# Kernel optimization log

Hardware: AMD Instinct MI355X
Metric: run time of the kernel (lower is better)

The kernel has to match this reference:

```python
import jax, jax.numpy as jnp
import numpy as np

N_NODES = 50000
N_EDGES = 400000
IN_F = 512
HID = 512      # 2 * out_features
OUT_F = 256
N_CELL = 1000
N_DIM = 128
N_SEL = 8192
N_C = 1024


def setup_inputs() -> dict:
    key = jax.random.key(0)
    ks = jax.random.split(key, 16)
    x = jax.random.normal(ks[0], (N_NODES, IN_F), dtype=jnp.float32)
    src = jax.random.randint(ks[1], (N_EDGES,), 0, N_NODES, dtype=jnp.int32)
    dst = jax.random.randint(ks[2], (N_EDGES,), 0, N_NODES, dtype=jnp.int32)
    x_indices = jax.random.randint(ks[3], (N_SEL,), 0, N_NODES, dtype=jnp.int32)
    c_indices = jax.random.randint(ks[4], (N_C,), 0, N_CELL, dtype=jnp.int32)
    s = lambda f: 1.0 / np.sqrt(f)
    W1 = jax.random.normal(ks[5], (IN_F, HID), dtype=jnp.float32) * s(IN_F)
    b1 = jnp.zeros((HID,), jnp.float32)
    W2 = jax.random.normal(ks[6], (HID, HID), dtype=jnp.float32) * s(HID)
    b2 = jnp.zeros((HID,), jnp.float32)
    W3 = jax.random.normal(ks[7], (HID, OUT_F), dtype=jnp.float32) * s(HID)
    b3 = jnp.zeros((OUT_F,), jnp.float32)
    Wp = jax.random.normal(ks[8], (OUT_F, N_DIM), dtype=jnp.float32) * s(OUT_F)
    bp = jnp.zeros((N_DIM,), jnp.float32)
    emb = jax.random.normal(ks[9], (N_CELL, N_DIM), dtype=jnp.float32)
    return {"x": x, "src": src, "dst": dst, "x_indices": x_indices,
            "c_indices": c_indices, "W1": W1, "b1": b1, "W2": W2, "b2": b2,
            "W3": W3, "b3": b3, "Wp": Wp, "bp": bp, "emb": emb}


def _degree_norms(src, dst, n):
    ones = jnp.ones(src.shape[0], jnp.float32)
    deg_out = jax.ops.segment_sum(ones, src, num_segments=n)
    deg_in = jax.ops.segment_sum(ones, dst, num_segments=n)
    ns = jnp.where(deg_out > 0, jax.lax.rsqrt(jnp.maximum(deg_out, 1.0)), 0.0)
    nd = jnp.where(deg_in > 0, jax.lax.rsqrt(jnp.maximum(deg_in, 1.0)), 0.0)
    return ns[:, None], nd[:, None]


def _gconv(h, src, dst, norm_src, norm_dst, W, b, n):
    # DGL GraphConv, norm='both': D_in^{-1/2} A D_out^{-1/2} H W + b
    msg = (h * norm_src)[src]                         # [E, F]
    agg = jax.ops.segment_sum(msg, dst, num_segments=n)
    return (agg * norm_dst) @ W + b


def reference(x, src, dst, x_indices, c_indices, W1, b1, W2, b2, W3, b3, Wp, bp, emb):
    n = x.shape[0]
    ns, nd = _degree_norms(src, dst, n)
    h = jax.nn.relu(_gconv(x, src, dst, ns, nd, W1, b1, n))
    h = jax.nn.relu(_gconv(h, src, dst, ns, nd, W2, b2, n))
    h = jax.nn.relu(_gconv(h, src, dst, ns, nd, W3, b3, n))
    enc = h[x_indices]                                # [N_SEL, OUT_F]
    proj = enc @ Wp + bp                              # Dropout in eval mode = identity
    e = emb[c_indices]                                # [N_C, N_DIM]
    return e @ proj.T                                 # [N_C, N_SEL]
```

## Files before the change

### kernel.cpp

```cpp
#include <hip/hip_runtime.h>

typedef unsigned int u32;
typedef unsigned short u16;

#define N_NODES 50000
#define N_EDGES 400000
#define IN_F 512
#define HID 512
#define OUT_F 256
#define N_CELL 1000
#define N_DIM 128
#define N_SEL 8192
#define N_C 1024
#define MPAD 50176

#define SCAN_B 256
#define SCAN_NB ((N_NODES + SCAN_B - 1) / SCAN_B)

typedef __bf16 bf16x8 __attribute__((ext_vector_type(8)));
typedef float f32x4 __attribute__((ext_vector_type(4)));

__device__ __forceinline__ u16 f2bf(float f) {
    u32 u = __builtin_bit_cast(u32, f);
    u32 r = (u + 0x7fffu + ((u >> 16) & 1u)) >> 16;
    return (u16)r;
}
__device__ __forceinline__ float bf2f(u32 bits16) {
    return __builtin_bit_cast(float, bits16 << 16);
}

__device__ __forceinline__ void async_copy16(const u16* g, u16* l) {
    __builtin_amdgcn_global_load_lds(
        (const __attribute__((address_space(1))) void*)g,
        (__attribute__((address_space(3))) void*)l, 16, 0, 0);
}


__global__ void degrees_kernel(const int* __restrict__ src, const int* __restrict__ dst,
                               int* __restrict__ degO, int* __restrict__ degI) {
    int e = blockIdx.x * 256 + threadIdx.x;
    if (e < N_EDGES) {
        atomicAdd(&degO[src[e]], 1);
        atomicAdd(&degI[dst[e]], 1);
    }
}

__global__ void scan_blocksum_kernel(const int* __restrict__ deg, int* __restrict__ bsum) {
    __shared__ int sh[SCAN_B];
    int i = blockIdx.x * SCAN_B + threadIdx.x;
    int v = (i < N_NODES) ? deg[i] : 0;
    sh[threadIdx.x] = v;
    __syncthreads();
    for (int off = SCAN_B / 2; off > 0; off >>= 1) {
        if (threadIdx.x < off) sh[threadIdx.x] += sh[threadIdx.x + off];
        __syncthreads();
    }
    if (threadIdx.x == 0) bsum[blockIdx.x] = sh[0];
}

__global__ void scan_bsum_kernel(const int* __restrict__ bsum, int* __restrict__ boff) {
    __shared__ int sh[SCAN_B];
    const int t = threadIdx.x;
    int v = (t < SCAN_NB) ? bsum[t] : 0;
    sh[t] = v;
    __syncthreads();
    for (int off = 1; off < SCAN_B; off <<= 1) {
        int u = (t >= off) ? sh[t - off] : 0;
        __syncthreads();
        sh[t] += u;
        __syncthreads();
    }
    if (t < SCAN_NB) boff[t] = sh[t] - v;
}

__global__ void scan_final_kernel(const int* __restrict__ deg, const int* __restrict__ boff,
                                  int* __restrict__ offs) {
    __shared__ int sh[SCAN_B];
    const int t = threadIdx.x;
    int i = blockIdx.x * SCAN_B + t;
    int v = (i < N_NODES) ? deg[i] : 0;
    sh[t] = v;
    __syncthreads();
    for (int off = 1; off < SCAN_B; off <<= 1) {
        int u = (t >= off) ? sh[t - off] : 0;
        __syncthreads();
        sh[t] += u;
        __syncthreads();
    }
    if (i < N_NODES) offs[i] = boff[blockIdx.x] + sh[t] - v;
    if (i == 0) offs[N_NODES] = N_EDGES;
}

__global__ void fill_csr_kernel(const int* __restrict__ src, const int* __restrict__ dst,
                                int* __restrict__ cursor, const int* __restrict__ offs,
                                int* __restrict__ csr) {
    int e = blockIdx.x * 256 + threadIdx.x;
    if (e < N_EDGES) {
        int d = dst[e];
        int slot = atomicAdd(&cursor[d], 1);
        csr[offs[d] + slot] = src[e];
    }
}

__global__ void norms_kernel(const int* __restrict__ degO, const int* __restrict__ degI,
                             float* __restrict__ ns, float* __restrict__ nd) {
    int i = blockIdx.x * 256 + threadIdx.x;
    if (i < N_NODES) {
        ns[i] = degO[i] > 0 ? rsqrtf((float)degO[i]) : 0.f;
        nd[i] = degI[i] > 0 ? rsqrtf((float)degI[i]) : 0.f;
    }
}


__global__ void trans_bf16_kernel(const float* __restrict__ src, u16* __restrict__ dst,
                                  int K, int N) {
    int i = blockIdx.x * 256 + threadIdx.x;
    if (i >= K * N) return;
    int n = i / K, k = i % K;
    dst[i] = f2bf(src[k * N + n]);
}

__global__ void convert_x_kernel(const float* __restrict__ x, u16* __restrict__ xb) {
    int i = blockIdx.x * 256 + threadIdx.x;
    int base = i * 4;
    int m = base >> 9;
    ushort4 o;
    if (m < N_NODES) {
        float4 v = *(const float4*)(x + base);
        o.x = f2bf(v.x); o.y = f2bf(v.y); o.z = f2bf(v.z); o.w = f2bf(v.w);
    } else {
        o = make_ushort4(0, 0, 0, 0);
    }
    *(ushort4*)(xb + base) = o;
}

__global__ void gather_emb_kernel(const float* __restrict__ emb, const int* __restrict__ cidx,
                                  u16* __restrict__ eb) {
    int c = blockIdx.x, f = threadIdx.x;
    eb[c * N_DIM + f] = f2bf(emb[(size_t)cidx[c] * N_DIM + f]);
}

__global__ __launch_bounds__(256, 4) void gemm_bf16_nt(
    const u16* __restrict__ A, const u16* __restrict__ B,
    const int* __restrict__ aidx,
    u16* __restrict__ Cb, float* __restrict__ Cf,
    const float* __restrict__ scale, int nScale,
    const float* __restrict__ bias,
    int N, int K) {
    __shared__ __align__(16) u16 As[2 * 4096];
    __shared__ __align__(16) u16 Bs[2 * 4096];
    const int t = threadIdx.x;
    const int m0 = blockIdx.x * 128, n0 = blockIdx.y * 128;
    const int l = t & 63, w = t >> 6;
    const int wm = (w >> 1) << 6, wn = (w & 1) << 6;
    const int lr = l & 15, quad = l >> 4;

    const int lrow = l >> 2;
    const int kof = (((l & 3) ^ ((l >> 3) & 3)) << 3);
    const int r0 = w, r1 = w + 4;
    int ar0 = m0 + r0 * 16 + lrow;
    int ar1 = m0 + r1 * 16 + lrow;
    if (aidx) { ar0 = aidx[ar0]; ar1 = aidx[ar1]; }
    const u16* gA0 = A + (size_t)ar0 * K + kof;
    const u16* gA1 = A + (size_t)ar1 * K + kof;
    const u16* gB0 = B + (size_t)(n0 + r0 * 16 + lrow) * K + kof;
    const u16* gB1 = B + (size_t)(n0 + r1 * 16 + lrow) * K + kof;
    u16* lA0 = As + r0 * 512;
    u16* lA1 = As + r1 * 512;
    u16* lB0 = Bs + r0 * 512;
    u16* lB1 = Bs + r1 * 512;

    f32x4 acc[4][4] = {};

    async_copy16(gA0, lA0);
    async_copy16(gA1, lA1);
    async_copy16(gB0, lB0);
    async_copy16(gB1, lB1);

    const int qoff = ((quad ^ ((l >> 1) & 3)) << 3);

    const int niter = K >> 5;
    for (int it = 0; it < niter; ++it) {
        const int cur = (it & 1) << 12;
        const int nxt = 4096 - cur;
        __syncthreads();
        if (it + 1 < niter) {
            const int ks = (it + 1) << 5;
            async_copy16(gA0 + ks, lA0 + nxt);
            async_copy16(gA1 + ks, lA1 + nxt);
            async_copy16(gB0 + ks, lB0 + nxt);
            async_copy16(gB1 + ks, lB1 + nxt);
        }
        bf16x8 af[4], bg[4];
#pragma unroll
        for (int i = 0; i < 4; ++i)
            af[i] = *(const bf16x8*)&As[cur + (wm + i * 16 + lr) * 32 + qoff];
#pragma unroll
        for (int j = 0; j < 4; ++j)
            bg[j] = *(const bf16x8*)&Bs[cur + (wn + j * 16 + lr) * 32 + qoff];
#pragma unroll
        for (int i = 0; i < 4; ++i)
#pragma unroll
            for (int j = 0; j < 4; ++j)
                acc[i][j] = __builtin_amdgcn_mfma_f32_16x16x32_bf16(af[i], bg[j], acc[i][j], 0, 0, 0);
    }

#pragma unroll
    for (int i = 0; i < 4; ++i) {
        int rbase = m0 + wm + i * 16 + quad * 4;
#pragma unroll
        for (int j = 0; j < 4; ++j) {
            int col = n0 + wn + j * 16 + lr;
            float bv = bias ? bias[col] : 0.f;
#pragma unroll
            for (int r = 0; r < 4; ++r) {
                int rg = rbase + r;
                float sc = scale ? (rg < nScale ? scale[rg] : 0.f) : 1.f;
                float v = acc[i][j][r] * sc + bv;
                if (Cb) Cb[(size_t)rg * N + col] = f2bf(v);
                else    Cf[(size_t)rg * N + col] = v;
            }
        }
    }
}

template <int W32>
struct AggVec;
template <> struct AggVec<4> { using T = uint4; };
template <> struct AggVec<2> { using T = uint2; };

template <int F>
__global__ __launch_bounds__(256) void aggregate_kernel(
    const u16* __restrict__ T, const int* __restrict__ csr,
    const int* __restrict__ offs, const float* __restrict__ nd,
    const float* __restrict__ bias, u16* __restrict__ H) {
    constexpr int W32 = F / 128;
    using VT = typename AggVec<W32>::T;
    const int t = threadIdx.x, w = t >> 6, l = t & 63;
    const int node = blockIdx.x * 4 + w;
    u32* __restrict__ Hrow = (u32*)H + (size_t)node * (F / 2) + l * W32;
    if (node >= N_NODES) {
        VT z = {};
        *(VT*)Hrow = z;
        return;
    }
    const int s0 = __builtin_amdgcn_readfirstlane(offs[node]);
    const int s1 = __builtin_amdgcn_readfirstlane(offs[node + 1]);
    const u32* __restrict__ Tb = (const u32*)T + l * W32;

    float acc[4][2 * W32];
#pragma unroll
    for (int c = 0; c < 4; ++c)
#pragma unroll
        for (int j = 0; j < 2 * W32; ++j) acc[c][j] = 0.f;

    int e = s0;
    for (; e + 8 <= s1; e += 8) {
        int si[8];
#pragma unroll
        for (int c = 0; c < 8; ++c) si[c] = csr[e + c];
        VT v[8];
#pragma unroll
        for (int c = 0; c < 8; ++c)
            v[c] = *(const VT*)(Tb + (size_t)si[c] * (F / 2));
#pragma unroll
        for (int c = 0; c < 8; ++c) {
            const u32* vv = (const u32*)&v[c];
#pragma unroll
            for (int j = 0; j < W32; ++j) {
                acc[c & 3][2 * j] += bf2f(vv[j] & 0xffffu);
                acc[c & 3][2 * j + 1] += bf2f(vv[j] >> 16);
            }
        }
    }
    for (; e + 4 <= s1; e += 4) {
        int si[4];
#pragma unroll
        for (int c = 0; c < 4; ++c) si[c] = csr[e + c];
        VT v[4];
#pragma unroll
        for (int c = 0; c < 4; ++c)
            v[c] = *(const VT*)(Tb + (size_t)si[c] * (F / 2));
#pragma unroll
        for (int c = 0; c < 4; ++c) {
            const u32* vv = (const u32*)&v[c];
#pragma unroll
            for (int j = 0; j < W32; ++j) {
                acc[c][2 * j] += bf2f(vv[j] & 0xffffu);
                acc[c][2 * j + 1] += bf2f(vv[j] >> 16);
            }
        }
    }
    for (; e < s1; ++e) {
        int s = csr[e];
        VT v = *(const VT*)(Tb + (size_t)s * (F / 2));
        const u32* vv = (const u32*)&v;
#pragma unroll
        for (int j = 0; j < W32; ++j) {
            acc[0][2 * j] += bf2f(vv[j] & 0xffffu);
            acc[0][2 * j + 1] += bf2f(vv[j] >> 16);
        }
    }

    const float ndv = nd[node];
    u32 ow[W32];
#pragma unroll
    for (int j = 0; j < W32; ++j) {
        float a0 = acc[0][2 * j] + acc[1][2 * j] + acc[2][2 * j] + acc[3][2 * j];
        float a1 = acc[0][2 * j + 1] + acc[1][2 * j + 1] + acc[2][2 * j + 1] + acc[3][2 * j + 1];
        float r0 = fmaxf(fmaf(a0, ndv, bias[l * 2 * W32 + 2 * j]), 0.f);
        float r1 = fmaxf(fmaf(a1, ndv, bias[l * 2 * W32 + 2 * j + 1]), 0.f);
        ow[j] = (u32)f2bf(r0) | ((u32)f2bf(r1) << 16);
    }
    VT o;
    u32* op = (u32*)&o;
#pragma unroll
    for (int j = 0; j < W32; ++j) op[j] = ow[j];
    *(VT*)Hrow = o;
}


extern "C" void kernel_launch(void* const* d_in, const int* in_sizes, int n_in,
                              void* d_out, int out_size, void* d_ws, size_t ws_size,
                              hipStream_t stream) {
    const float* x   = (const float*)d_in[0];
    const int*   src = (const int*)d_in[1];
    const int*   dst = (const int*)d_in[2];
    const int*   xidx= (const int*)d_in[3];
    const int*   cidx= (const int*)d_in[4];
    const float* W1  = (const float*)d_in[5];
    const float* b1  = (const float*)d_in[6];
    const float* W2  = (const float*)d_in[7];
    const float* b2  = (const float*)d_in[8];
    const float* W3  = (const float*)d_in[9];
    const float* b3  = (const float*)d_in[10];
    const float* Wp  = (const float*)d_in[11];
    const float* bp  = (const float*)d_in[12];
    const float* emb = (const float*)d_in[13];
    float* out = (float*)d_out;

    char* p = (char*)d_ws;
    auto alloc = [&](size_t bytes) {
        char* r = p;
        p += (bytes + 255) & ~(size_t)255;
        return r;
    };
    u16* T    = (u16*)alloc((size_t)MPAD * 512 * 2);
    u16* HX   = (u16*)alloc((size_t)MPAD * 512 * 2);
    u16* W1T  = (u16*)alloc((size_t)512 * 512 * 2);
    u16* W2T  = (u16*)alloc((size_t)512 * 512 * 2);
    u16* W3T  = (u16*)alloc((size_t)256 * 512 * 2);
    u16* WpT  = (u16*)alloc((size_t)128 * 256 * 2);
    u16* projb= (u16*)alloc((size_t)N_SEL * N_DIM * 2);
    u16* eb   = (u16*)alloc((size_t)N_C * N_DIM * 2);
    int* degO   = (int*)alloc(N_NODES * 4);
    int* degI   = (int*)alloc(N_NODES * 4);
    int* cursor = (int*)alloc(N_NODES * 4);
    int* offs   = (int*)alloc((N_NODES + 1) * 4);
    float* ns   = (float*)alloc(N_NODES * 4);
    float* nd   = (float*)alloc(N_NODES * 4);
    int* csr    = (int*)alloc(N_EDGES * 4);
    int* bsum   = (int*)alloc(SCAN_NB * 4);
    int* boff   = (int*)alloc(SCAN_NB * 4);
    if ((size_t)(p - (char*)d_ws) > ws_size) return;

    hipMemsetAsync(degO, 0, (size_t)((char*)offs - (char*)degO), stream);
    degrees_kernel<<<(N_EDGES + 255) / 256, 256, 0, stream>>>(src, dst, degO, degI);
    scan_blocksum_kernel<<<SCAN_NB, SCAN_B, 0, stream>>>(degI, bsum);
    scan_bsum_kernel<<<1, SCAN_B, 0, stream>>>(bsum, boff);
    scan_final_kernel<<<SCAN_NB, SCAN_B, 0, stream>>>(degI, boff, offs);
    fill_csr_kernel<<<(N_EDGES + 255) / 256, 256, 0, stream>>>(src, dst, cursor, offs, csr);
    norms_kernel<<<(N_NODES + 255) / 256, 256, 0, stream>>>(degO, degI, ns, nd);

    trans_bf16_kernel<<<(512 * 512) / 256, 256, 0, stream>>>(W1, W1T, 512, 512);
    trans_bf16_kernel<<<(512 * 512) / 256, 256, 0, stream>>>(W2, W2T, 512, 512);
    trans_bf16_kernel<<<(512 * 256) / 256, 256, 0, stream>>>(W3, W3T, 512, 256);
    trans_bf16_kernel<<<(256 * 128) / 256, 256, 0, stream>>>(Wp, WpT, 256, 128);
    convert_x_kernel<<<(MPAD * 512 / 4) / 256, 256, 0, stream>>>(x, HX);
    gather_emb_kernel<<<N_C, N_DIM, 0, stream>>>(emb, cidx, eb);

    gemm_bf16_nt<<<dim3(MPAD / 128, 512 / 128), 256, 0, stream>>>(
        HX, W1T, nullptr, T, nullptr, ns, N_NODES, nullptr, 512, 512);
    aggregate_kernel<512><<<MPAD / 4, 256, 0, stream>>>(T, csr, offs, nd, b1, HX);
    gemm_bf16_nt<<<dim3(MPAD / 128, 512 / 128), 256, 0, stream>>>(
        HX, W2T, nullptr, T, nullptr, ns, N_NODES, nullptr, 512, 512);
    aggregate_kernel<512><<<MPAD / 4, 256, 0, stream>>>(T, csr, offs, nd, b2, HX);
    gemm_bf16_nt<<<dim3(MPAD / 128, 256 / 128), 256, 0, stream>>>(
        HX, W3T, nullptr, T, nullptr, ns, N_NODES, nullptr, 256, 512);
    aggregate_kernel<256><<<MPAD / 4, 256, 0, stream>>>(T, csr, offs, nd, b3, HX);

    gemm_bf16_nt<<<dim3(N_SEL / 128, 1), 256, 0, stream>>>(
        HX, WpT, xidx, projb, nullptr, nullptr, 0, bp, N_DIM, 256);
    gemm_bf16_nt<<<dim3(N_C / 128, N_SEL / 128), 256, 0, stream>>>(
        eb, projb, nullptr, nullptr, out, nullptr, 0, nullptr, N_SEL, N_DIM);
}
```

Before: 597.2 us.

## Compute third GCN layer only for selected nodes via aggregate-then-transform

The third graph convolution is now evaluated only for the 8192 selected rows. The second aggregation pre-scales its output by the source norm. A new kernel gathers and aggregates 512-wide neighbour rows for each selected node, and only then multiplies by W3 with bias and ReLU fused into the GEMM epilogue. This drops the full 50k-row layer-3 GEMM and aggregation, at the cost of aggregating at width 512 instead of 256 for the selected nodes. The existing xidx gather in the projection GEMM is removed.

```diff
diff --git a/kernel.cpp b/kernel.cpp
--- a/kernel.cpp
+++ b/kernel.cpp
@@ -145,7 +145,7 @@
     const int* __restrict__ aidx,
     u16* __restrict__ Cb, float* __restrict__ Cf,
     const float* __restrict__ scale, int nScale,
-    const float* __restrict__ bias,
+    const float* __restrict__ bias, int doRelu,
     int N, int K) {
     __shared__ __align__(16) u16 As[2 * 4096];
     __shared__ __align__(16) u16 Bs[2 * 4096];
@@ -217,6 +217,7 @@
                 int rg = rbase + r;
                 float sc = scale ? (rg < nScale ? scale[rg] : 0.f) : 1.f;
                 float v = acc[i][j][r] * sc + bv;
+                if (doRelu) v = fmaxf(v, 0.f);
                 if (Cb) Cb[(size_t)rg * N + col] = f2bf(v);
                 else    Cf[(size_t)rg * N + col] = v;
             }
@@ -233,7 +234,8 @@
 __global__ __launch_bounds__(256) void aggregate_kernel(
     const u16* __restrict__ T, const int* __restrict__ csr,
     const int* __restrict__ offs, const float* __restrict__ nd,
-    const float* __restrict__ bias, u16* __restrict__ H) {
+    const float* __restrict__ bias, const float* __restrict__ nsOut,
+    u16* __restrict__ H) {
     constexpr int W32 = F / 128;
     using VT = typename AggVec<W32>::T;
     const int t = threadIdx.x, w = t >> 6, l = t & 63;
@@ -303,13 +305,14 @@
     }
 
     const float ndv = nd[node];
+    const float nsv = nsOut ? nsOut[node] : 1.f;
     u32 ow[W32];
 #pragma unroll
     for (int j = 0; j < W32; ++j) {
         float a0 = acc[0][2 * j] + acc[1][2 * j] + acc[2][2 * j] + acc[3][2 * j];
         float a1 = acc[0][2 * j + 1] + acc[1][2 * j + 1] + acc[2][2 * j + 1] + acc[3][2 * j + 1];
-        float r0 = fmaxf(fmaf(a0, ndv, bias[l * 2 * W32 + 2 * j]), 0.f);
-        float r1 = fmaxf(fmaf(a1, ndv, bias[l * 2 * W32 + 2 * j + 1]), 0.f);
+        float r0 = fmaxf(fmaf(a0, ndv, bias[l * 2 * W32 + 2 * j]), 0.f) * nsv;
+        float r1 = fmaxf(fmaf(a1, ndv, bias[l * 2 * W32 + 2 * j + 1]), 0.f) * nsv;
         ow[j] = (u32)f2bf(r0) | ((u32)f2bf(r1) << 16);
     }
     VT o;
@@ -317,6 +320,84 @@
 #pragma unroll
     for (int j = 0; j < W32; ++j) op[j] = ow[j];
     *(VT*)Hrow = o;
+}
+
+__global__ __launch_bounds__(256) void aggregate_sel_kernel(
+    const u16* __restrict__ Tn, const int* __restrict__ csr,
+    const int* __restrict__ offs, const float* __restrict__ nd,
+    const int* __restrict__ xidx, u16* __restrict__ S) {
+    const int t = threadIdx.x, w = t >> 6, l = t & 63;
+    const int slot = blockIdx.x * 4 + w;
+    const int node = __builtin_amdgcn_readfirstlane(xidx[slot]);
+    const int s0 = __builtin_amdgcn_readfirstlane(offs[node]);
+    const int s1 = __builtin_amdgcn_readfirstlane(offs[node + 1]);
+    const u32* __restrict__ Tb = (const u32*)Tn + l * 4;
+    u32* __restrict__ Srow = (u32*)S + (size_t)slot * 256 + l * 4;
+
+    float acc[4][8];
+#pragma unroll
+    for (int c = 0; c < 4; ++c)
+#pragma unroll
+        for (int j = 0; j < 8; ++j) acc[c][j] = 0.f;
+
+    int e = s0;
+    for (; e + 8 <= s1; e += 8) {
+        int si[8];
+#pragma unroll
+        for (int c = 0; c < 8; ++c) si[c] = csr[e + c];
+        uint4 v[8];
+#pragma unroll
+        for (int c = 0; c < 8; ++c)
+            v[c] = *(const uint4*)(Tb + (size_t)si[c] * 256);
+#pragma unroll
+        for (int c = 0; c < 8; ++c) {
+            const u32* vv = (const u32*)&v[c];
+#pragma unroll
+            for (int j = 0; j < 4; ++j) {
+                acc[c & 3][2 * j] += bf2f(vv[j] & 0xffffu);
+                acc[c & 3][2 * j + 1] += bf2f(vv[j] >> 16);
+            }
+        }
+    }
+    for (; e + 4 <= s1; e += 4) {
+        int si[4];
+#pragma unroll
+        for (int c = 0; c < 4; ++c) si[c] = csr[e + c];
+        uint4 v[4];
+#pragma unroll
+        for (int c = 0; c < 4; ++c)
+            v[c] = *(const uint4*)(Tb + (size_t)si[c] * 256);
+#pragma unroll
+        for (int c = 0; c < 4; ++c) {
+            const u32* vv = (const u32*)&v[c];
+#pragma unroll
+            for (int j = 0; j < 4; ++j) {
+                acc[c][2 * j] += bf2f(vv[j] & 0xffffu);
+                acc[c][2 * j + 1] += bf2f(vv[j] >> 16);
+            }
+        }
+    }
+    for (; e < s1; ++e) {
+        int s = csr[e];
+        uint4 v = *(const uint4*)(Tb + (size_t)s * 256);
+        const u32* vv = (const u32*)&v;
+#pragma unroll
+        for (int j = 0; j < 4; ++j) {
+            acc[0][2 * j] += bf2f(vv[j] & 0xffffu);
+            acc[0][2 * j + 1] += bf2f(vv[j] >> 16);
+        }
+    }
+
+    const float ndv = nd[node];
+    uint4 o;
+    u32* op = (u32*)&o;
+#pragma unroll
+    for (int j = 0; j < 4; ++j) {
+        float a0 = (acc[0][2 * j] + acc[1][2 * j] + acc[2][2 * j] + acc[3][2 * j]) * ndv;
+        float a1 = (acc[0][2 * j + 1] + acc[1][2 * j + 1] + acc[2][2 * j + 1] + acc[3][2 * j + 1]) * ndv;
+        op[j] = (u32)f2bf(a0) | ((u32)f2bf(a1) << 16);
+    }
+    *(uint4*)Srow = o;
 }
 
 
@@ -351,6 +432,8 @@
     u16* W2T  = (u16*)alloc((size_t)512 * 512 * 2);
     u16* W3T  = (u16*)alloc((size_t)256 * 512 * 2);
     u16* WpT  = (u16*)alloc((size_t)128 * 256 * 2);
+    u16* Ssel = (u16*)alloc((size_t)N_SEL * 512 * 2);
+    u16* encb = (u16*)alloc((size_t)N_SEL * OUT_F * 2);
     u16* projb= (u16*)alloc((size_t)N_SEL * N_DIM * 2);
     u16* eb   = (u16*)alloc((size_t)N_C * N_DIM * 2);
     int* degO   = (int*)alloc(N_NODES * 4);
@@ -380,17 +463,17 @@
     gather_emb_kernel<<<N_C, N_DIM, 0, stream>>>(emb, cidx, eb);
 
     gemm_bf16_nt<<<dim3(MPAD / 128, 512 / 128), 256, 0, stream>>>(
-        HX, W1T, nullptr, T, nullptr, ns, N_NODES, nullptr, 512, 512);
-    aggregate_kernel<512><<<MPAD / 4, 256, 0, stream>>>(T, csr, offs, nd, b1, HX);
+        HX, W1T, nullptr, T, nullptr, ns, N_NODES, nullptr, 0, 512, 512);
+    aggregate_kernel<512><<<MPAD / 4, 256, 0, stream>>>(T, csr, offs, nd, b1, nullptr, HX);
     gemm_bf16_nt<<<dim3(MPAD / 128, 512 / 128), 256, 0, stream>>>(
-        HX, W2T, nullptr, T, nullptr, ns, N_NODES, nullptr, 512, 512);
-    aggregate_kernel<512><<<MPAD / 4, 256, 0, stream>>>(T, csr, offs, nd, b2, HX);
-    gemm_bf16_nt<<<dim3(MPAD / 128, 256 / 128), 256, 0, stream>>>(
-        HX, W3T, nullptr, T, nullptr, ns, N_NODES, nullptr, 256, 512);
-    aggregate_kernel<256><<<MPAD / 4, 256, 0, stream>>>(T, csr, offs, nd, b3, HX);
+        HX, W2T, nullptr, T, nullptr, ns, N_NODES, nullptr, 0, 512, 512);
+    aggregate_kernel<512><<<MPAD / 4, 256, 0, stream>>>(T, csr, offs, nd, b2, ns, HX);
+    aggregate_sel_kernel<<<N_SEL / 4, 256, 0, stream>>>(HX, csr, offs, nd, xidx, Ssel);
+    gemm_bf16_nt<<<dim3(N_SEL / 128, 256 / 128), 256, 0, stream>>>(
+        Ssel, W3T, nullptr, encb, nullptr, nullptr, 0, b3, 1, 256, 512);
 
     gemm_bf16_nt<<<dim3(N_SEL / 128, 1), 256, 0, stream>>>(
-        HX, WpT, xidx, projb, nullptr, nullptr, 0, bp, N_DIM, 256);
+        encb, WpT, nullptr, projb, nullptr, nullptr, 0, bp, 0, N_DIM, 256);
     gemm_bf16_nt<<<dim3(N_C / 128, N_SEL / 128), 256, 0, stream>>>(
-        eb, projb, nullptr, nullptr, out, nullptr, 0, nullptr, N_SEL, N_DIM);
-}
+        eb, projb, nullptr, nullptr, out, nullptr, 0, nullptr, 0, N_SEL, N_DIM);
+}
```

Result: faster. 578.8 us (-3.1%).
